# Optimization experiments

Hardware: AMD Instinct MI355X
Metric: run time of the kernel (lower is better)

## Reference

```python
import jax, jax.numpy as jnp
import numpy as np

MB, E, N, IN_HALF, HID, OUT = 32, 4, 512, 64, 128, 128
EPS = 1e-5


def setup_inputs() -> dict:
    key = jax.random.key(0)
    ks = jax.random.split(key, 24)
    x = jax.random.normal(ks[0], (MB, N, IN_HALF), jnp.float32)
    u = jax.random.uniform(ks[1], (MB, E, N, N), jnp.float32)
    a = (u < 0.02).astype(jnp.float32)
    adj = jnp.maximum(a, jnp.swapaxes(a, -1, -2))  # symmetric 0/1, forward's sym branch holds
    def lin(k, i, o):
        return jax.random.normal(k, (i, o), jnp.float32) / np.float32(np.sqrt(i))
    d = {"x": x, "adj": adj}
    in_dims = [IN_HALF, HID, HID]
    for l in range(3):
        d[f"w_self{l}"] = lin(ks[2 + 6 * l], in_dims[l], HID)
        d[f"b_self{l}"] = jnp.zeros((HID,), jnp.float32)
        d[f"w_edge{l}"] = lin(ks[3 + 6 * l], in_dims[l], HID * E)
        d[f"b_edge{l}"] = jnp.zeros((HID * E,), jnp.float32)
        d[f"bn{l}_g"] = jnp.ones((N,), jnp.float32)
        d[f"bn{l}_b"] = jnp.zeros((N,), jnp.float32)
    d["w1"] = lin(ks[20], HID, HID)
    d["b1"] = jnp.zeros((HID,), jnp.float32)
    d["bn_f_g"] = jnp.ones((N,), jnp.float32)
    d["bn_f_b"] = jnp.zeros((N,), jnp.float32)
    d["w2"] = lin(ks[21], HID, OUT)
    d["b2"] = jnp.zeros((OUT,), jnp.float32)
    return d


def _rescale_adj(adj):
    # zero the diagonal, then normalize each column by total neighbor count
    n = adj.shape[-1]
    adj = adj * (1.0 - jnp.eye(n, dtype=adj.dtype))
    deg = adj.sum(axis=(1, 2))  # (mb, N): sum over edge types and rows
    inv = jnp.where(deg > 0, 1.0 / deg, 0.0)
    return inv[:, None, None, :] * adj


def _batchnorm_nodes(h, g, b):
    # torch BatchNorm1d(n_node) on (B, N, D): per-node stats over (B, D), biased var
    m = h.mean(axis=(0, 2), keepdims=True)
    v = ((h - m) ** 2).mean(axis=(0, 2), keepdims=True)
    return (h - m) / jnp.sqrt(v + EPS) * g[None, :, None] + b[None, :, None]


def _graph_conv(h, na, w_self, b_self, w_edge, b_edge):
    mb, n, _ = h.shape
    hs = h @ w_self + b_self  # (mb, N, out)
    m = (h @ w_edge + b_edge).reshape(mb, n, HID, E)  # (mb, N, out, E)
    # fused: per-edge-type adj matmul + sum over edge types, no (mb,E,N,out) blowup
    hr = jnp.einsum('benm,bmoe->bno', na, m)
    return hs + hr


def reference(x, adj,
              w_self0, b_self0, w_edge0, b_edge0, bn0_g, bn0_b,
              w_self1, b_self1, w_edge1, b_edge1, bn1_g, bn1_b,
              w_self2, b_self2, w_edge2, b_edge2, bn2_g, bn2_b,
              w1, b1, bn_f_g, bn_f_b, w2, b2):
    # adj is symmetric by construction -> forward's adj_sym == adj
    na = _rescale_adj(adj)  # identical across layers; computed once
    h = x
    layers = [
        (w_self0, b_self0, w_edge0, b_edge0, bn0_g, bn0_b),
        (w_self1, b_self1, w_edge1, b_edge1, bn1_g, bn1_b),
        (w_self2, b_self2, w_edge2, b_edge2, bn2_g, bn2_b),
    ]
    for ws, bs, we, be, g, b in layers:
        h = _graph_conv(h, na, ws, bs, we, be)
        h = _batchnorm_nodes(h, g, b)
        h = jax.nn.relu(h)
    h = h @ w1 + b1
    h = _batchnorm_nodes(h, bn_f_g, bn_f_b)
    h = jax.nn.relu(h)
    h = h @ w2 + b2
    return h
```

## Files before the change

kernel.cpp:

```cpp
#include <hip/hip_runtime.h>
#include <stdint.h>


typedef float  f32x4  __attribute__((ext_vector_type(4)));
typedef __bf16 bf16x8 __attribute__((ext_vector_type(8)));
typedef __bf16 bf16x4 __attribute__((ext_vector_type(4)));
typedef unsigned short ushort8v __attribute__((ext_vector_type(8)));
typedef uint32_t uint4v __attribute__((ext_vector_type(4)));

#define MBATCH 32
#define ETYPES 4
#define NNODE  512
#define HIDD   128

#define GLB(p) (const __attribute__((address_space(1))) uint32_t*)(p)
#define LDSp(p) (__attribute__((address_space(3))) uint32_t*)(p)

#define WP_S0 0
#define WP_E0 8192
#define WP_S1 40960
#define WP_E1 57344
#define WP_S2 122880
#define WP_E2 139264
#define WP_W1 204800
#define WP_W2 221184

struct Params {
  const float* x;
  const float* adj;
  const float* wself[3]; const float* bself[3];
  const float* wedge[3]; const float* bedge[3];
  const float* bng[3];   const float* bnb[3];
  const float* w1; const float* b1;
  const float* bnfg; const float* bnfb;
  const float* w2; const float* b2;
  __bf16* mmp; float* hs; __bf16* part;
  __bf16* hb0; __bf16* hb1;
  uint32_t* bm; float* degp; __bf16* wp;
  float* out;
};

__device__ void pack_phase(const float* __restrict__ adj, uint32_t* __restrict__ bm,
                           float* __restrict__ degp, int bid, int t, int nbl) {
  int wave = t >> 6, lane = t & 63;
  for (int rg = bid; rg < 16384; rg += nbl) {
    int r = rg * 4 + wave;
    int b = r >> 11, e = (r >> 9) & 3, n = r & 511;
    const float* row = adj + (long)r * 512;
    uint32_t myw = 0;
#pragma unroll
    for (int i = 0; i < 8; ++i) {
      uint64_t bal = __ballot(row[i * 64 + lane] != 0.f);
      uint32_t lo = (uint32_t)bal, hi = (uint32_t)(bal >> 32);
      if ((lane >> 1) == i) myw = (lane & 1) ? hi : lo;
    }
    if (lane == (n >> 5)) myw &= ~(1u << (n & 31));
    int pc = (lane < 16) ? __popc(myw) : 0;
    pc += __shfl_down(pc, 8);
    pc += __shfl_down(pc, 4);
    pc += __shfl_down(pc, 2);
    pc += __shfl_down(pc, 1);
    if (lane < 16) bm[(long)r * 16 + lane] = myw;
    if (lane == 0) degp[e * 16384 + b * 512 + n] = (float)pc;
  }
}

__device__ void prep_phase(const Params& P, int bid, int t, int nbl) {
  const float* Ws[8] = {P.wself[0], P.wedge[0], P.wself[1], P.wedge[1],
                        P.wself[2], P.wedge[2], P.w1, P.w2};
  const int Kt[8]  = {64, 64, 128, 128, 128, 128, 128, 128};
  const int NB[8]  = {2, 8, 2, 8, 2, 8, 2, 2};
  const int OFF[8] = {WP_S0, WP_E0, WP_S1, WP_E1, WP_S2, WP_E2, WP_W1, WP_W2};
#pragma unroll
  for (int wid = 0; wid < 8; ++wid) {
    int K = Kt[wid], nblk = NB[wid];
    int tot = K * nblk * 64;
    for (int gid = bid * 256 + t; gid < tot; gid += nbl * 256) {
      int c = gid & 63;
      int k = (gid >> 6) % K;
      int blk = (gid >> 6) / K;
      int edge = (nblk == 8);
      int WS = edge ? 512 : 128;
      int col = edge ? (((blk & 1) * 64 + c) * 4 + (blk >> 1)) : (blk * 64 + c);
      P.wp[OFF[wid] + (long)blk * K * 64 + (k >> 3) * 512 + c * 8 + (k & 7)] =
          (__bf16)Ws[wid][k * WS + col];
    }
  }
}

template <int K, bool F32IN>
__device__ void gemm_phase(char* smem, const void* __restrict__ hv,
                           const __bf16* __restrict__ wp_self,
                           const float* __restrict__ bias_self,
                           const __bf16* __restrict__ wp_edge,
                           const float* __restrict__ bias_edge,
                           const float* __restrict__ degp,
                           float* __restrict__ outF, __bf16* __restrict__ mmp,
                           int ntiles, int bid, int t, int nbl) {
  __bf16 (*Hl)[K + 8] = (__bf16(*)[K + 8])smem;
  __bf16* Wl = (__bf16*)(smem + 64 * (K + 8) * 2);
  int wave = t >> 6, lane = t & 63, l15 = lane & 15, q = lane >> 4;
  for (int tile = bid; tile < ntiles; tile += nbl) {
    __syncthreads();
    int g0 = (tile & 255) * 64;
    int by = tile >> 8;
    bool edge = by >= 2;
    {
      const __bf16* wblk = edge ? (wp_edge + (long)(by - 2) * K * 64)
                                : (wp_self + (long)by * K * 64);
      const char* g = (const char*)wblk;
#pragma unroll
      for (int i = 0; i < K / 32; ++i) {
        __builtin_amdgcn_global_load_lds(GLB(g + i * 4096 + wave * 1024 + lane * 16),
                                         LDSp((char*)Wl + i * 4096 + wave * 1024),
                                         16, 0, 0);
      }
    }
    for (int idx = t; idx < 64 * (K / 8); idx += 256) {
      int r = idx / (K / 8), ch = idx % (K / 8);
      if (F32IN) {
        const float* xf = (const float*)hv;
        f32x4 a = *(const f32x4*)(xf + (long)(g0 + r) * K + ch * 8);
        f32x4 bq = *(const f32x4*)(xf + (long)(g0 + r) * K + ch * 8 + 4);
        bf16x8 o;
#pragma unroll
        for (int j = 0; j < 4; ++j) { o[j] = (__bf16)a[j]; o[4 + j] = (__bf16)bq[j]; }
        *(bf16x8*)&Hl[r][ch * 8] = o;
      } else {
        const __bf16* hb = (const __bf16*)hv;
        *(bf16x8*)&Hl[r][ch * 8] = *(const bf16x8*)(hb + (long)(g0 + r) * K + ch * 8);
      }
    }
    __syncthreads();
    f32x4 acc[4] = {};
#pragma unroll
    for (int kk = 0; kk < K / 32; ++kk) {
      bf16x8 af = *(const bf16x8*)&Hl[wave * 16 + l15][kk * 32 + q * 8];
#pragma unroll
      for (int c = 0; c < 4; ++c) {
        bf16x8 bfr = *(const bf16x8*)&Wl[((kk * 4 + q) * 64 + c * 16 + l15) * 8];
        acc[c] = __builtin_amdgcn_mfma_f32_16x16x32_bf16(af, bfr, acc[c], 0, 0, 0);
      }
    }
    if (!edge) {
      int c0 = by * 64;
#pragma unroll
      for (int c = 0; c < 4; ++c) {
        float bc = bias_self[c0 + c * 16 + l15];
#pragma unroll
        for (int i = 0; i < 4; ++i) {
          int g = g0 + wave * 16 + q * 4 + i;
          outF[(long)g * HIDD + c0 + c * 16 + l15] = acc[c][i] + bc;
        }
      }
    } else {
      int blk = by - 2;
      int e = blk >> 1, o0 = (blk & 1) * 64;
      float iv[4];
#pragma unroll
      for (int i = 0; i < 4; ++i) {
        int gg = g0 + wave * 16 + q * 4 + i;
        float d = degp[gg] + degp[16384 + gg] + degp[32768 + gg] + degp[49152 + gg];
        iv[i] = d > 0.f ? 1.f / d : 0.f;
      }
      int b4e  = (g0 >> 9) * 4 + e;
      int octg = ((g0 & 511) >> 3) + wave * 2 + (q >> 1);
      int j0   = (q & 1) * 4;
#pragma unroll
      for (int c = 0; c < 4; ++c) {
        int o = o0 + c * 16 + l15;
        float bc = bias_edge[o * 4 + e];
        bf16x4 v4;
#pragma unroll
        for (int i = 0; i < 4; ++i) v4[i] = (__bf16)((acc[c][i] + bc) * iv[i]);
        *(bf16x4*)(mmp + ((long)(b4e * 64 + octg) * HIDD + o) * 8 + j0) = v4;
      }
    }
  }
}

__device__ void spmm_phase(char* smem, const uint32_t* __restrict__ bm,
                           const __bf16* __restrict__ mmp,
                           __bf16* __restrict__ part, int bid, int t) {
  int wave = t >> 6, lane = t & 63, l15 = lane & 15, q = lane >> 4;
  int tile = bid >> 7;
  int eb   = bid & 127;
  int e = eb >> 5, b = eb & 31;
  int nt = tile >> 1, oc = tile & 1;
  int n0 = nt * 128, o0 = oc * 64;

  const uint32_t* bmr = bm + ((long)((b * 4 + e) * 512 + n0 + wave * 32 + l15)) * 16;
  uint32_t rm0[16], rm1[16];
#pragma unroll
  for (int i = 0; i < 4; ++i) {
    uint4v v0 = *(const uint4v*)(bmr + i * 4);
    uint4v v1 = *(const uint4v*)(bmr + 256 + i * 4);
    rm0[i * 4 + 0] = v0.x; rm0[i * 4 + 1] = v0.y; rm0[i * 4 + 2] = v0.z; rm0[i * 4 + 3] = v0.w;
    rm1[i * 4 + 0] = v1.x; rm1[i * 4 + 1] = v1.y; rm1[i * 4 + 2] = v1.z; rm1[i * 4 + 3] = v1.w;
  }

  auto stage = [&](int mc, char* dst) {
#pragma unroll
    for (int i = 0; i < 2; ++i) {
      int oct = wave * 2 + i;
      const char* g = (const char*)mmp +
          ((long)(b * 4 + e) * 65536 + mc * 8192 + oct * 1024 + o0 * 8) * 2;
      __builtin_amdgcn_global_load_lds(GLB(g + lane * 16),
                                       LDSp(dst + oct * 1024), 16, 0, 0);
    }
  };

  stage(0, smem);
  stage(1, smem + 8192);
  stage(2, smem + 16384);

  f32x4 acc0[4] = {}, acc1[4] = {};
#pragma unroll
  for (int mc = 0; mc < 8; ++mc) {
    if (mc <= 5)      asm volatile("s_waitcnt vmcnt(4)" ::: "memory");
    else if (mc == 6) asm volatile("s_waitcnt vmcnt(2)" ::: "memory");
    else              asm volatile("s_waitcnt vmcnt(0)" ::: "memory");
    __builtin_amdgcn_s_barrier();
    asm volatile("" ::: "memory");
    if (mc < 5) stage(mc + 3, smem + ((mc + 3) & 3) * 8192);
    const __bf16* Bl = (const __bf16*)(smem + (mc & 3) * 8192);
#pragma unroll
    for (int kk = 0; kk < 2; ++kk) {
      uint32_t bits0 = (rm0[mc * 2 + kk] >> (q * 8)) & 0xffu;
      uint32_t bits1 = (rm1[mc * 2 + kk] >> (q * 8)) & 0xffu;
      ushort8v a0, a1;
#pragma unroll
      for (int j = 0; j < 8; ++j) {
        a0[j] = (bits0 >> j & 1u) ? (unsigned short)0x3F80 : (unsigned short)0;
        a1[j] = (bits1 >> j & 1u) ? (unsigned short)0x3F80 : (unsigned short)0;
      }
      union { ushort8v u; bf16x8 v; } c0, c1; c0.u = a0; c1.u = a1;
#pragma unroll
      for (int c = 0; c < 4; ++c) {
        bf16x8 bfr = *(const bf16x8*)&Bl[((kk * 4 + q) * 64 + c * 16 + l15) * 8];
        acc0[c] = __builtin_amdgcn_mfma_f32_16x16x32_bf16(c0.v, bfr, acc0[c], 0, 0, 0);
        acc1[c] = __builtin_amdgcn_mfma_f32_16x16x32_bf16(c1.v, bfr, acc1[c], 0, 0, 0);
      }
    }
  }

  __bf16* dst = part + (long)(e * 32 + b) * NNODE * HIDD;
#pragma unroll
  for (int c = 0; c < 4; ++c) {
#pragma unroll
    for (int i = 0; i < 4; ++i) {
      int n = n0 + wave * 32 + q * 4 + i;
      int o = o0 + c * 16 + l15;
      dst[(long)n * HIDD + o] = (__bf16)acc0[c][i];
      dst[(long)(n + 16) * HIDD + o] = (__bf16)acc1[c][i];
    }
  }
}

template <bool HASP>
__device__ void bnstat_phase(char* smem, const float* __restrict__ hs,
                             const __bf16* __restrict__ part,
                             const float* __restrict__ gg,
                             const float* __restrict__ bb,
                             __bf16* __restrict__ hb, int bid, int t, int nbl) {
  float* sm = (float*)smem;
  float* rs = (float*)(smem + 16384);
  float* rq = (float*)(smem + 17408);
  float* bc = (float*)(smem + 18432);
  int o4 = t & 31, bq = t >> 5;
  for (int n = bid; n < 512; n += nbl) {
    __syncthreads();
    float s = 0.f, sq = 0.f;
#pragma unroll
    for (int i = 0; i < 4; ++i) {
      int b = bq + i * 8;
      long base = ((long)b * NNODE + n) * HIDD + o4 * 4;
      f32x4 v = *(const f32x4*)(hs + base);
      if (HASP) {
#pragma unroll
        for (int e = 0; e < 4; ++e) {
          bf16x4 pv = *(const bf16x4*)(part + ((long)(e * 32 + b) * NNODE + n) * HIDD + o4 * 4);
#pragma unroll
          for (int j = 0; j < 4; ++j) v[j] += (float)pv[j];
        }
      }
      *(f32x4*)&sm[b * 128 + o4 * 4] = v;
#pragma unroll
      for (int j = 0; j < 4; ++j) { s += v[j]; sq += v[j] * v[j]; }
    }
    rs[t] = s; rq[t] = sq;
    __syncthreads();
    for (int off = 128; off > 0; off >>= 1) {
      if (t < off) { rs[t] += rs[t + off]; rq[t] += rq[t + off]; }
      __syncthreads();
    }
    if (t == 0) {
      float mean = rs[0] * (1.f / 4096.f);
      float var = rq[0] * (1.f / 4096.f) - mean * mean;
      float rstd = rsqrtf(var + 1e-5f);
      float sc = gg[n] * rstd;
      bc[0] = sc;
      bc[1] = bb[n] - mean * sc;
    }
    __syncthreads();
    float sc = bc[0], sh = bc[1];
#pragma unroll
    for (int i = 0; i < 4; ++i) {
      int b = bq + i * 8;
      f32x4 v = *(const f32x4*)&sm[b * 128 + o4 * 4];
      bf16x4 o;
#pragma unroll
      for (int j = 0; j < 4; ++j) {
        float x = v[j] * sc + sh;
        o[j] = (__bf16)(x > 0.f ? x : 0.f);
      }
      *(bf16x4*)(hb + ((long)b * NNODE + n) * HIDD + o4 * 4) = o;
    }
  }
}

__global__ __launch_bounds__(256) void g_packprep(Params P) {
  pack_phase(P.adj, P.bm, P.degp, blockIdx.x, threadIdx.x, gridDim.x);
  prep_phase(P, blockIdx.x, threadIdx.x, gridDim.x);
}
template <int K, bool F32IN>
__global__ __launch_bounds__(256) void g_gemm(const void* hv, const __bf16* wps,
                                              const float* bs, const __bf16* wpe,
                                              const float* be, const float* degp,
                                              float* outF, __bf16* mmp, int ntiles) {
  __shared__ __align__(16) char smem[64 * (K + 8) * 2 + K * 64 * 2];
  gemm_phase<K, F32IN>(smem, hv, wps, bs, wpe, be, degp, outF, mmp, ntiles,
                       blockIdx.x, threadIdx.x, gridDim.x);
}
__global__ __launch_bounds__(256) void g_spmm(const uint32_t* bm, const __bf16* mmp,
                                              __bf16* part) {
  __shared__ __align__(16) char smem[32768];
  spmm_phase(smem, bm, mmp, part, blockIdx.x, threadIdx.x);
}
template <bool HASP>
__global__ __launch_bounds__(256) void g_bnstat(const float* hs, const __bf16* part,
                                                const float* gg, const float* bb,
                                                __bf16* hb) {
  __shared__ __align__(16) char smem[18448];
  bnstat_phase<HASP>(smem, hs, part, gg, bb, hb, blockIdx.x, threadIdx.x, gridDim.x);
}

extern "C" void kernel_launch(void* const* d_in, const int* in_sizes, int n_in,
                              void* d_out, int out_size, void* d_ws, size_t ws_size,
                              hipStream_t stream) {
  (void)in_sizes; (void)n_in; (void)out_size; (void)ws_size;
  Params P;
  P.x   = (const float*)d_in[0];
  P.adj = (const float*)d_in[1];
  for (int l = 0; l < 3; ++l) {
    P.wself[l] = (const float*)d_in[2 + 6 * l];
    P.bself[l] = (const float*)d_in[3 + 6 * l];
    P.wedge[l] = (const float*)d_in[4 + 6 * l];
    P.bedge[l] = (const float*)d_in[5 + 6 * l];
    P.bng[l]   = (const float*)d_in[6 + 6 * l];
    P.bnb[l]   = (const float*)d_in[7 + 6 * l];
  }
  P.w1   = (const float*)d_in[20];
  P.b1   = (const float*)d_in[21];
  P.bnfg = (const float*)d_in[22];
  P.bnfb = (const float*)d_in[23];
  P.w2   = (const float*)d_in[24];
  P.b2   = (const float*)d_in[25];

  char* ws = (char*)d_ws;
  P.mmp  = (__bf16*)ws;
  P.hs   = (float*)(ws + 16777216);
  P.part = (__bf16*)(ws + 25165824);
  P.hb0  = (__bf16*)(ws + 41943040);
  P.hb1  = (__bf16*)(ws + 46137344);
  P.bm   = (uint32_t*)(ws + 50331648);
  P.degp = (float*)(ws + 54525952);
  P.wp   = (__bf16*)(ws + 54788096);
  P.out  = (float*)d_out;

  g_packprep<<<16384, 256, 0, stream>>>(P);

  g_gemm<64, true><<<2560, 256, 0, stream>>>(P.x, P.wp + WP_S0, P.bself[0],
                                             P.wp + WP_E0, P.bedge[0], P.degp,
                                             P.hs, P.mmp, 2560);
  g_spmm<<<1024, 256, 0, stream>>>(P.bm, P.mmp, P.part);
  g_bnstat<true><<<512, 256, 0, stream>>>(P.hs, P.part, P.bng[0], P.bnb[0], P.hb0);

  g_gemm<128, false><<<2560, 256, 0, stream>>>(P.hb0, P.wp + WP_S1, P.bself[1],
                                               P.wp + WP_E1, P.bedge[1], P.degp,
                                               P.hs, P.mmp, 2560);
  g_spmm<<<1024, 256, 0, stream>>>(P.bm, P.mmp, P.part);
  g_bnstat<true><<<512, 256, 0, stream>>>(P.hs, P.part, P.bng[1], P.bnb[1], P.hb1);

  g_gemm<128, false><<<2560, 256, 0, stream>>>(P.hb1, P.wp + WP_S2, P.bself[2],
                                               P.wp + WP_E2, P.bedge[2], P.degp,
                                               P.hs, P.mmp, 2560);
  g_spmm<<<1024, 256, 0, stream>>>(P.bm, P.mmp, P.part);
  g_bnstat<true><<<512, 256, 0, stream>>>(P.hs, P.part, P.bng[2], P.bnb[2], P.hb0);

  g_gemm<128, false><<<512, 256, 0, stream>>>(P.hb0, P.wp + WP_W1, P.b1,
                                              nullptr, nullptr, P.degp,
                                              P.hs, nullptr, 512);
  g_bnstat<false><<<512, 256, 0, stream>>>(P.hs, nullptr, P.bnfg, P.bnfb, P.hb1);
  g_gemm<128, false><<<512, 256, 0, stream>>>(P.hb1, P.wp + WP_W2, P.b2,
                                              nullptr, nullptr, P.degp,
                                              P.out, nullptr, 512);
}
```

Before: 351.7 us.

## Fuse final batchnorm into w1/w2 GEMMs and vectorize adjacency bit packing

The final BatchNorm is folded into the GEMMs. The w1 GEMM writes bf16 output and accumulates per-node sum and sum-of-squares with atomics. The w2 GEMM then applies scale, shift and ReLU while loading its input tile, which removes one bnstat launch and its extra pass over memory. Separately, adjacency packing now reads rows as vectorized float4 loads and assembles the bitmask with shuffles instead of eight ballots. The fused path computes variance as E[x²]−mean², which is less numerically stable, and the atomics run in nondeterministic order.

```diff
diff --git a/kernel.cpp b/kernel.cpp
--- a/kernel.cpp
+++ b/kernel.cpp
@@ -36,7 +36,7 @@
   const float* w2; const float* b2;
   __bf16* mmp; float* hs; __bf16* part;
   __bf16* hb0; __bf16* hb1;
-  uint32_t* bm; float* degp; __bf16* wp;
+  uint32_t* bm; float* degp; __bf16* wp; float* stats;
   float* out;
 };
 
@@ -47,13 +47,19 @@
     int r = rg * 4 + wave;
     int b = r >> 11, e = (r >> 9) & 3, n = r & 511;
     const float* row = adj + (long)r * 512;
-    uint32_t myw = 0;
-#pragma unroll
-    for (int i = 0; i < 8; ++i) {
-      uint64_t bal = __ballot(row[i * 64 + lane] != 0.f);
-      uint32_t lo = (uint32_t)bal, hi = (uint32_t)(bal >> 32);
-      if ((lane >> 1) == i) myw = (lane & 1) ? hi : lo;
-    }
+    f32x4 a  = *(const f32x4*)(row + lane * 8);
+    f32x4 bv = *(const f32x4*)(row + lane * 8 + 4);
+    uint32_t byt = 0;
+#pragma unroll
+    for (int j = 0; j < 4; ++j) {
+      byt |= (a[j]  != 0.f ? 1u : 0u) << j;
+      byt |= (bv[j] != 0.f ? 1u : 0u) << (4 + j);
+    }
+    uint32_t tv = __shfl_xor(byt, 1);
+    byt = (lane & 1) ? ((byt << 8) | tv) : (byt | (tv << 8));
+    tv = __shfl_xor(byt, 2);
+    byt = (lane & 2) ? ((byt << 16) | tv) : (byt | (tv << 16));
+    uint32_t myw = __shfl(byt, (lane & 15) << 2);
     if (lane == (n >> 5)) myw &= ~(1u << (n & 31));
     int pc = (lane < 16) ? __popc(myw) : 0;
     pc += __shfl_down(pc, 8);
@@ -88,23 +94,39 @@
   }
 }
 
-template <int K, bool F32IN>
+template <int K, int INM, int OUTM>
 __device__ void gemm_phase(char* smem, const void* __restrict__ hv,
+                           const float* __restrict__ stin,
+                           const float* __restrict__ bg,
+                           const float* __restrict__ bb,
                            const __bf16* __restrict__ wp_self,
                            const float* __restrict__ bias_self,
                            const __bf16* __restrict__ wp_edge,
                            const float* __restrict__ bias_edge,
                            const float* __restrict__ degp,
-                           float* __restrict__ outF, __bf16* __restrict__ mmp,
+                           float* __restrict__ outF, __bf16* __restrict__ outB,
+                           float* __restrict__ stout,
+                           __bf16* __restrict__ mmp,
                            int ntiles, int bid, int t, int nbl) {
   __bf16 (*Hl)[K + 8] = (__bf16(*)[K + 8])smem;
   __bf16* Wl = (__bf16*)(smem + 64 * (K + 8) * 2);
+  float* scsh = (float*)(smem + 64 * (K + 8) * 2 + K * 64 * 2);
   int wave = t >> 6, lane = t & 63, l15 = lane & 15, q = lane >> 4;
   for (int tile = bid; tile < ntiles; tile += nbl) {
-    __syncthreads();
     int g0 = (tile & 255) * 64;
     int by = tile >> 8;
     bool edge = by >= 2;
+    if (INM == 2 && t < 64) {
+      int n = (g0 + t) & 511;
+      float s = stin[n * 2], sq = stin[n * 2 + 1];
+      float mean = s * (1.f / 4096.f);
+      float var = sq * (1.f / 4096.f) - mean * mean;
+      float rstd = rsqrtf(var + 1e-5f);
+      float sc = bg[n] * rstd;
+      scsh[t * 2] = sc;
+      scsh[t * 2 + 1] = bb[n] - mean * sc;
+    }
+    __syncthreads();
     {
       const __bf16* wblk = edge ? (wp_edge + (long)(by - 2) * K * 64)
                                 : (wp_self + (long)by * K * 64);
@@ -118,7 +140,7 @@
     }
     for (int idx = t; idx < 64 * (K / 8); idx += 256) {
       int r = idx / (K / 8), ch = idx % (K / 8);
-      if (F32IN) {
+      if (INM == 0) {
         const float* xf = (const float*)hv;
         f32x4 a = *(const f32x4*)(xf + (long)(g0 + r) * K + ch * 8);
         f32x4 bq = *(const f32x4*)(xf + (long)(g0 + r) * K + ch * 8 + 4);
@@ -126,9 +148,20 @@
 #pragma unroll
         for (int j = 0; j < 4; ++j) { o[j] = (__bf16)a[j]; o[4 + j] = (__bf16)bq[j]; }
         *(bf16x8*)&Hl[r][ch * 8] = o;
-      } else {
+      } else if (INM == 1) {
         const __bf16* hb = (const __bf16*)hv;
         *(bf16x8*)&Hl[r][ch * 8] = *(const bf16x8*)(hb + (long)(g0 + r) * K + ch * 8);
+      } else {
+        float sc = scsh[r * 2], sh = scsh[r * 2 + 1];
+        const __bf16* hbp = (const __bf16*)hv;
+        bf16x8 hvv = *(const bf16x8*)(hbp + (long)(g0 + r) * K + ch * 8);
+        bf16x8 o;
+#pragma unroll
+        for (int j = 0; j < 8; ++j) {
+          float x = (float)hvv[j] * sc + sh;
+          o[j] = (__bf16)(x > 0.f ? x : 0.f);
+        }
+        *(bf16x8*)&Hl[r][ch * 8] = o;
       }
     }
     __syncthreads();
@@ -144,13 +177,43 @@
     }
     if (!edge) {
       int c0 = by * 64;
-#pragma unroll
-      for (int c = 0; c < 4; ++c) {
-        float bc = bias_self[c0 + c * 16 + l15];
+      if (OUTM == 0) {
+#pragma unroll
+        for (int c = 0; c < 4; ++c) {
+          float bc = bias_self[c0 + c * 16 + l15];
+#pragma unroll
+          for (int i = 0; i < 4; ++i) {
+            int g = g0 + wave * 16 + q * 4 + i;
+            outF[(long)g * HIDD + c0 + c * 16 + l15] = acc[c][i] + bc;
+          }
+        }
+      } else {
+        float rs[4] = {}, rq[4] = {};
+#pragma unroll
+        for (int c = 0; c < 4; ++c) {
+          float bc = bias_self[c0 + c * 16 + l15];
+#pragma unroll
+          for (int i = 0; i < 4; ++i) {
+            int g = g0 + wave * 16 + q * 4 + i;
+            float x = acc[c][i] + bc;
+            __bf16 xb = (__bf16)x;
+            outB[(long)g * HIDD + c0 + c * 16 + l15] = xb;
+            float rv = (float)xb;
+            rs[i] += rv; rq[i] += rv * rv;
+          }
+        }
 #pragma unroll
         for (int i = 0; i < 4; ++i) {
-          int g = g0 + wave * 16 + q * 4 + i;
-          outF[(long)g * HIDD + c0 + c * 16 + l15] = acc[c][i] + bc;
+          float s = rs[i], sq = rq[i];
+          s += __shfl_xor(s, 1); s += __shfl_xor(s, 2);
+          s += __shfl_xor(s, 4); s += __shfl_xor(s, 8);
+          sq += __shfl_xor(sq, 1); sq += __shfl_xor(sq, 2);
+          sq += __shfl_xor(sq, 4); sq += __shfl_xor(sq, 8);
+          if (l15 == 0) {
+            int n = (g0 + wave * 16 + q * 4 + i) & 511;
+            atomicAdd(&stout[n * 2], s);
+            atomicAdd(&stout[n * 2 + 1], sq);
+          }
         }
       }
     } else {
@@ -257,7 +320,6 @@
   }
 }
 
-template <bool HASP>
 __device__ void bnstat_phase(char* smem, const float* __restrict__ hs,
                              const __bf16* __restrict__ part,
                              const float* __restrict__ gg,
@@ -276,13 +338,11 @@
       int b = bq + i * 8;
       long base = ((long)b * NNODE + n) * HIDD + o4 * 4;
       f32x4 v = *(const f32x4*)(hs + base);
-      if (HASP) {
-#pragma unroll
-        for (int e = 0; e < 4; ++e) {
-          bf16x4 pv = *(const bf16x4*)(part + ((long)(e * 32 + b) * NNODE + n) * HIDD + o4 * 4);
-#pragma unroll
-          for (int j = 0; j < 4; ++j) v[j] += (float)pv[j];
-        }
+#pragma unroll
+      for (int e = 0; e < 4; ++e) {
+        bf16x4 pv = *(const bf16x4*)(part + ((long)(e * 32 + b) * NNODE + n) * HIDD + o4 * 4);
+#pragma unroll
+        for (int j = 0; j < 4; ++j) v[j] += (float)pv[j];
       }
       *(f32x4*)&sm[b * 128 + o4 * 4] = v;
 #pragma unroll
@@ -320,29 +380,35 @@
 }
 
 __global__ __launch_bounds__(256) void g_packprep(Params P) {
+  if (blockIdx.x == 0) {
+    for (int i = threadIdx.x; i < 1024; i += 256) P.stats[i] = 0.f;
+  }
   pack_phase(P.adj, P.bm, P.degp, blockIdx.x, threadIdx.x, gridDim.x);
   prep_phase(P, blockIdx.x, threadIdx.x, gridDim.x);
 }
-template <int K, bool F32IN>
-__global__ __launch_bounds__(256) void g_gemm(const void* hv, const __bf16* wps,
-                                              const float* bs, const __bf16* wpe,
-                                              const float* be, const float* degp,
-                                              float* outF, __bf16* mmp, int ntiles) {
-  __shared__ __align__(16) char smem[64 * (K + 8) * 2 + K * 64 * 2];
-  gemm_phase<K, F32IN>(smem, hv, wps, bs, wpe, be, degp, outF, mmp, ntiles,
-                       blockIdx.x, threadIdx.x, gridDim.x);
+template <int K, int INM, int OUTM>
+__global__ __launch_bounds__(256) void g_gemm(const void* hv, const float* stin,
+                                              const float* bg, const float* bb,
+                                              const __bf16* wps, const float* bs,
+                                              const __bf16* wpe, const float* be,
+                                              const float* degp, float* outF,
+                                              __bf16* outB, float* stout,
+                                              __bf16* mmp, int ntiles) {
+  __shared__ __align__(16) char smem[64 * (K + 8) * 2 + K * 64 * 2 + 512];
+  gemm_phase<K, INM, OUTM>(smem, hv, stin, bg, bb, wps, bs, wpe, be, degp,
+                           outF, outB, stout, mmp, ntiles,
+                           blockIdx.x, threadIdx.x, gridDim.x);
 }
 __global__ __launch_bounds__(256) void g_spmm(const uint32_t* bm, const __bf16* mmp,
                                               __bf16* part) {
   __shared__ __align__(16) char smem[32768];
   spmm_phase(smem, bm, mmp, part, blockIdx.x, threadIdx.x);
 }
-template <bool HASP>
 __global__ __launch_bounds__(256) void g_bnstat(const float* hs, const __bf16* part,
                                                 const float* gg, const float* bb,
                                                 __bf16* hb) {
   __shared__ __align__(16) char smem[18448];
-  bnstat_phase<HASP>(smem, hs, part, gg, bb, hb, blockIdx.x, threadIdx.x, gridDim.x);
+  bnstat_phase(smem, hs, part, gg, bb, hb, blockIdx.x, threadIdx.x, gridDim.x);
 }
 
 extern "C" void kernel_launch(void* const* d_in, const int* in_sizes, int n_in,
@@ -368,41 +434,41 @@
   P.b2   = (const float*)d_in[25];
 
   char* ws = (char*)d_ws;
-  P.mmp  = (__bf16*)ws;
-  P.hs   = (float*)(ws + 16777216);
-  P.part = (__bf16*)(ws + 25165824);
-  P.hb0  = (__bf16*)(ws + 41943040);
-  P.hb1  = (__bf16*)(ws + 46137344);
-  P.bm   = (uint32_t*)(ws + 50331648);
-  P.degp = (float*)(ws + 54525952);
-  P.wp   = (__bf16*)(ws + 54788096);
-  P.out  = (float*)d_out;
+  P.mmp   = (__bf16*)ws;
+  P.hs    = (float*)(ws + 16777216);
+  P.part  = (__bf16*)(ws + 25165824);
+  P.hb0   = (__bf16*)(ws + 41943040);
+  P.hb1   = (__bf16*)(ws + 46137344);
+  P.bm    = (uint32_t*)(ws + 50331648);
+  P.degp  = (float*)(ws + 54525952);
+  P.wp    = (__bf16*)(ws + 54788096);
+  P.stats = (float*)(ws + 55263232);
+  P.out   = (float*)d_out;
 
   g_packprep<<<16384, 256, 0, stream>>>(P);
 
-  g_gemm<64, true><<<2560, 256, 0, stream>>>(P.x, P.wp + WP_S0, P.bself[0],
-                                             P.wp + WP_E0, P.bedge[0], P.degp,
-                                             P.hs, P.mmp, 2560);
+  g_gemm<64, 0, 0><<<2560, 256, 0, stream>>>(P.x, nullptr, nullptr, nullptr,
+      P.wp + WP_S0, P.bself[0], P.wp + WP_E0, P.bedge[0], P.degp,
+      P.hs, nullptr, nullptr, P.mmp, 2560);
   g_spmm<<<1024, 256, 0, stream>>>(P.bm, P.mmp, P.part);
-  g_bnstat<true><<<512, 256, 0, stream>>>(P.hs, P.part, P.bng[0], P.bnb[0], P.hb0);
-
-  g_gemm<128, false><<<2560, 256, 0, stream>>>(P.hb0, P.wp + WP_S1, P.bself[1],
-                                               P.wp + WP_E1, P.bedge[1], P.degp,
-                                               P.hs, P.mmp, 2560);
+  g_bnstat<<<512, 256, 0, stream>>>(P.hs, P.part, P.bng[0], P.bnb[0], P.hb0);
+
+  g_gemm<128, 1, 0><<<2560, 256, 0, stream>>>(P.hb0, nullptr, nullptr, nullptr,
+      P.wp + WP_S1, P.bself[1], P.wp + WP_E1, P.bedge[1], P.degp,
+      P.hs, nullptr, nullptr, P.mmp, 2560);
   g_spmm<<<1024, 256, 0, stream>>>(P.bm, P.mmp, P.part);
-  g_bnstat<true><<<512, 256, 0, stream>>>(P.hs, P.part, P.bng[1], P.bnb[1], P.hb1);
-
-  g_gemm<128, false><<<2560, 256, 0, stream>>>(P.hb1, P.wp + WP_S2, P.bself[2],
-                                               P.wp + WP_E2, P.bedge[2], P.degp,
-                                               P.hs, P.mmp, 2560);
+  g_bnstat<<<512, 256, 0, stream>>>(P.hs, P.part, P.bng[1], P.bnb[1], P.hb1);
+
+  g_gemm<128, 1, 0><<<2560, 256, 0, stream>>>(P.hb1, nullptr, nullptr, nullptr,
+      P.wp + WP_S2, P.bself[2], P.wp + WP_E2, P.bedge[2], P.degp,
+      P.hs, nullptr, nullptr, P.mmp, 2560);
   g_spmm<<<1024, 256, 0, stream>>>(P.bm, P.mmp, P.part);
-  g_bnstat<true><<<512, 256, 0, stream>>>(P.hs, P.part, P.bng[2], P.bnb[2], P.hb0);
-
-  g_gemm<128, false><<<512, 256, 0, stream>>>(P.hb0, P.wp + WP_W1, P.b1,
-                                              nullptr, nullptr, P.degp,
-                                              P.hs, nullptr, 512);
-  g_bnstat<false><<<512, 256, 0, stream>>>(P.hs, nullptr, P.bnfg, P.bnfb, P.hb1);
-  g_gemm<128, false><<<512, 256, 0, stream>>>(P.hb1, P.wp + WP_W2, P.b2,
-                                              nullptr, nullptr, P.degp,
-                                              P.out, nullptr, 512);
-}
+  g_bnstat<<<512, 256, 0, stream>>>(P.hs, P.part, P.bng[2], P.bnb[2], P.hb0);
+
+  g_gemm<128, 1, 1><<<512, 256, 0, stream>>>(P.hb0, nullptr, nullptr, nullptr,
+      P.wp + WP_W1, P.b1, nullptr, nullptr, P.degp,
+      nullptr, P.hb1, P.stats, nullptr, 512);
+  g_gemm<128, 2, 0><<<512, 256, 0, stream>>>(P.hb1, P.stats, P.bnfg, P.bnfb,
+      P.wp + WP_W2, P.b2, nullptr, nullptr, P.degp,
+      P.out, nullptr, nullptr, nullptr, 512);
+}
```

After: 359.5 us. +2.2%, slower.
